# Kernel optimization log

Hardware: AMD Instinct MI355X
Metric: run time of the kernel (lower is better)

## Reference

```python
import jax, jax.numpy as jnp
import numpy as np

B = 64          # decode batch (one token per sequence)
HID = 4096      # hidden_size
HQ = 32         # num query heads
HKV = 8         # num kv heads (GQA, groups = 4)
D = 128         # head_dim
BS = 16         # block_size of paged KV cache
MAXB = 64       # max blocks per sequence -> max context 1024
MAXPOS = 4096   # rope table length
TOTAL_SLOTS = B * MAXB * BS


def setup_inputs() -> dict:
    key = jax.random.key(0)
    ks = jax.random.split(key, 10)
    hidden = jax.random.normal(ks[0], (B, 1, HID), jnp.float32)
    context_lens = jax.random.randint(ks[1], (B,), 512, BS * MAXB + 1).astype(jnp.int32)
    positions = (context_lens - 1).reshape(B, 1)  # decoding token position
    # each sequence owns a contiguous range of blocks
    block_tables = jnp.arange(B * MAXB, dtype=jnp.int32).reshape(B, MAXB)
    last = context_lens - 1
    slot_mapping = (block_tables[jnp.arange(B), last // BS] * BS + last % BS).astype(jnp.int32)
    inv_freq = 1.0 / (10000.0 ** (jnp.arange(0, D, 2, dtype=jnp.float32) / D))
    freqs = jnp.outer(jnp.arange(MAXPOS, dtype=jnp.float32), inv_freq)  # [MAXPOS, D/2]
    cos, sin = jnp.cos(freqs), jnp.sin(freqs)
    key_cache = jax.random.normal(ks[2], (TOTAL_SLOTS, HKV, D), jnp.float32) * 0.5
    value_cache = jax.random.normal(ks[3], (TOTAL_SLOTS, HKV, D), jnp.float32) * 0.5
    Wq = jax.random.normal(ks[4], (HQ * D, HID), jnp.float32) * 0.02
    Wk = jax.random.normal(ks[5], (HKV * D, HID), jnp.float32) * 0.02
    Wv = jax.random.normal(ks[6], (HKV * D, HID), jnp.float32) * 0.02
    Wo = jax.random.normal(ks[7], (HID, HQ * D), jnp.float32) * 0.02
    return dict(hidden=hidden, positions=positions, cos=cos, sin=sin,
                key_cache=key_cache, value_cache=value_cache,
                slot_mapping=slot_mapping, block_tables=block_tables,
                context_lens=context_lens, Wq=Wq, Wk=Wk, Wv=Wv, Wo=Wo)


def reference(hidden, positions, cos, sin, key_cache, value_cache,
              slot_mapping, block_tables, context_lens, Wq, Wk, Wv, Wo):
    b, s, _ = hidden.shape  # s == 1 (paged decode path)
    q = (hidden @ Wq.T).reshape(b, s, HQ, D)
    k = (hidden @ Wk.T).reshape(b, s, HKV, D)
    v = (hidden @ Wv.T).reshape(b, s, HKV, D)
    # rotary embedding (half-split convention)
    c = cos[positions][:, :, None, :]  # [b,s,1,D/2]
    sn = sin[positions][:, :, None, :]
    def rope(x):
        x1, x2 = jnp.split(x, 2, axis=-1)
        return jnp.concatenate([x1 * c - x2 * sn, x2 * c + x1 * sn], axis=-1)
    q, k = rope(q), rope(k)
    # scatter current token's K/V into the paged cache via slot_mapping
    kc = key_cache.at[slot_mapping].set(k.reshape(-1, HKV, D))
    vc = value_cache.at[slot_mapping].set(v.reshape(-1, HKV, D))
    # gather each sequence's KV via block tables
    T = MAXB * BS
    t = jnp.arange(T)
    slots = block_tables[:, t // BS] * BS + (t % BS)  # [b, T]
    keys = kc[slots]   # [b, T, HKV, D]
    vals = vc[slots]   # [b, T, HKV, D]
    # GQA attention, q has one token per sequence
    G = HQ // HKV
    qg = q.reshape(b, HKV, G, D)
    scores = jnp.einsum('bkgd,btkd->bkgt', qg, keys) / jnp.sqrt(jnp.float32(D))
    mask = t[None, :] < context_lens[:, None]  # [b, T]
    scores = jnp.where(mask[:, None, None, :], scores, -jnp.inf)
    p = jax.nn.softmax(scores, axis=-1)
    out = jnp.einsum('bkgt,btkd->bkgd', p, vals).reshape(b, 1, HQ * D)
    return out @ Wo.T
```

## Files before the change

### kernel.cpp

```cpp
#include <hip/hip_runtime.h>
#include <hip/hip_bf16.h>

#define B_    64
#define HID_  4096
#define HQ_   32
#define HKV_  8
#define D_    128
#define BS_   16
#define MAXB_ 64

#define KS      16
#define KCHUNK  (HID_ / KS)
#define QKV_ROWS 6144
#define O_ROWS   4096
#define SPLITS  16

#define REGION_SZ ((size_t)KS * QKV_ROWS * 64)
#define QKVF_SZ  ((size_t)64 * 6144)
#define XB_SZ    ((size_t)HID_ * 64)

typedef __attribute__((ext_vector_type(8))) short bf16x8;
typedef __attribute__((ext_vector_type(4))) float f32x4;

__device__ inline unsigned short f2bf(float x) {
  __hip_bfloat16 h = __float2bfloat16(x);
  union { __hip_bfloat16 b; unsigned short u; } v; v.b = h;
  return v.u;
}
__device__ inline float bf2f(unsigned short h) {
  union { float f; unsigned u; } v; v.u = ((unsigned)h) << 16;
  return v.f;
}

__global__ __launch_bounds__(256) void convert_x(
    const float* __restrict__ X, unsigned short* __restrict__ XBhi,
    unsigned short* __restrict__ XBlo)
{
  int idx = blockIdx.x * 256 + threadIdx.x;
  int kg = idx >> 6, b = idx & 63;
  const float* xp = X + (size_t)b * HID_ + kg * 8;
  float4 a = *(const float4*)xp, c = *(const float4*)(xp + 4);
  float xs[8] = {a.x, a.y, a.z, a.w, c.x, c.y, c.z, c.w};
  unsigned short hi[8], lo[8];
  #pragma unroll
  for (int j = 0; j < 8; ++j) {
    hi[j] = f2bf(xs[j]);
    lo[j] = f2bf(xs[j] - bf2f(hi[j]));
  }
  *(uint4*)(XBhi + (size_t)idx * 8) = *(const uint4*)hi;
  *(uint4*)(XBlo + (size_t)idx * 8) = *(const uint4*)lo;
}

__global__ __launch_bounds__(256, 4) void gemm_mfma(
    const float* __restrict__ W0, const float* __restrict__ W1,
    const float* __restrict__ W2,
    const unsigned short* __restrict__ XBhi,
    const unsigned short* __restrict__ XBlo,
    int split1, int split2, int rows_total, float* __restrict__ part)
{
  const int tid = threadIdx.x;
  const int l   = tid & 63;
  const int w   = tid >> 6;
  const int r0  = blockIdx.x * 128 + w * 32;
  const int k0  = blockIdx.y * KCHUNK;

  const float* W; int rloc;
  if (r0 < split1)      { W = W0; rloc = r0; }
  else if (r0 < split2) { W = W1; rloc = r0 - split1; }
  else                  { W = W2; rloc = r0 - split2; }

  const int lm = l & 15;
  const int lk = l >> 4;

  const float* wp0 = W + (size_t)(rloc + lm) * HID_ + k0 + lk * 8;
  const float* wp1 = wp0 + (size_t)16 * HID_;
  const unsigned short* bh = XBhi + ((size_t)(k0 / 8 + lk) * 64 + lm) * 8;
  const unsigned short* bl = XBlo + ((size_t)(k0 / 8 + lk) * 64 + lm) * 8;

  f32x4 acc[2][4];
  #pragma unroll
  for (int rt = 0; rt < 2; ++rt)
    #pragma unroll
    for (int ct = 0; ct < 4; ++ct)
      #pragma unroll
      for (int i = 0; i < 4; ++i) acc[rt][ct][i] = 0.f;

  #pragma unroll 4
  for (int ks = 0; ks < KCHUNK / 32; ++ks) {
    bf16x8 Bh[4], Bl[4];
    #pragma unroll
    for (int ct = 0; ct < 4; ++ct) {
      Bh[ct] = *(const bf16x8*)(bh + (size_t)ks * 2048 + ct * 128);
      Bl[ct] = *(const bf16x8*)(bl + (size_t)ks * 2048 + ct * 128);
    }
    #pragma unroll
    for (int rt = 0; rt < 2; ++rt) {
      const float* wp = (rt ? wp1 : wp0) + ks * 32;
      float4 a0 = *(const float4*)wp;
      float4 a1 = *(const float4*)(wp + 4);
      float xs[8] = {a0.x, a0.y, a0.z, a0.w, a1.x, a1.y, a1.z, a1.w};
      bf16x8 Ah, Al;
      #pragma unroll
      for (int j = 0; j < 8; ++j) {
        unsigned short h = f2bf(xs[j]);
        Ah[j] = (short)h;
        Al[j] = (short)f2bf(xs[j] - bf2f(h));
      }
      #pragma unroll
      for (int ct = 0; ct < 4; ++ct) {
        acc[rt][ct] = __builtin_amdgcn_mfma_f32_16x16x32_bf16(Ah, Bh[ct], acc[rt][ct], 0, 0, 0);
        acc[rt][ct] = __builtin_amdgcn_mfma_f32_16x16x32_bf16(Al, Bh[ct], acc[rt][ct], 0, 0, 0);
        acc[rt][ct] = __builtin_amdgcn_mfma_f32_16x16x32_bf16(Ah, Bl[ct], acc[rt][ct], 0, 0, 0);
      }
    }
  }

  #pragma unroll
  for (int rt = 0; rt < 2; ++rt)
    #pragma unroll
    for (int ct = 0; ct < 4; ++ct) {
      int row = r0 + rt * 16 + lk * 4;
      int bat = ct * 16 + lm;
      #pragma unroll
      for (int i = 0; i < 4; ++i)
        part[((size_t)blockIdx.y * rows_total + row + i) * 64 + bat] = acc[rt][ct][i];
    }
}

__global__ __launch_bounds__(256) void reduce_rope(
    const float* __restrict__ part, const float* __restrict__ cosT,
    const float* __restrict__ sinT, const int* __restrict__ positions,
    float* __restrict__ qkvf)
{
  const int bb  = threadIdx.x & 63;
  const int cid = blockIdx.x * 4 + (threadIdx.x >> 6);
  const int pos = positions[bb];

  if (cid < 2048) {
    const int hq = cid >> 6, d0 = cid & 63;
    const int r1 = hq * 128 + d0;
    float x1 = 0.f, x2 = 0.f;
    #pragma unroll 8
    for (int ks = 0; ks < KS; ++ks) {
      x1 += part[((size_t)ks * QKV_ROWS + r1) * 64 + bb];
      x2 += part[((size_t)ks * QKV_ROWS + r1 + 64) * 64 + bb];
    }
    float c = cosT[pos * 64 + d0], s = sinT[pos * 64 + d0];
    const float scale = 0.08838834764831843f;
    qkvf[(size_t)(bb * 32 + hq) * 128 + d0]      = (x1 * c - x2 * s) * scale;
    qkvf[(size_t)(bb * 32 + hq) * 128 + d0 + 64] = (x2 * c + x1 * s) * scale;
  } else if (cid < 2560) {
    const int c2 = cid - 2048;
    const int kh = c2 >> 6, d0 = c2 & 63;
    const int r1 = 4096 + kh * 128 + d0;
    float x1 = 0.f, x2 = 0.f;
    #pragma unroll 8
    for (int ks = 0; ks < KS; ++ks) {
      x1 += part[((size_t)ks * QKV_ROWS + r1) * 64 + bb];
      x2 += part[((size_t)ks * QKV_ROWS + r1 + 64) * 64 + bb];
    }
    float c = cosT[pos * 64 + d0], s = sinT[pos * 64 + d0];
    qkvf[262144 + (size_t)(bb * 8 + kh) * 128 + d0]      = x1 * c - x2 * s;
    qkvf[262144 + (size_t)(bb * 8 + kh) * 128 + d0 + 64] = x2 * c + x1 * s;
  } else {
    const int c2 = cid - 2560;
    const int kh = c2 >> 6, d0 = c2 & 63;
    const int r1 = 5120 + kh * 128 + d0;
    float x1 = 0.f, x2 = 0.f;
    #pragma unroll 8
    for (int ks = 0; ks < KS; ++ks) {
      x1 += part[((size_t)ks * QKV_ROWS + r1) * 64 + bb];
      x2 += part[((size_t)ks * QKV_ROWS + r1 + 64) * 64 + bb];
    }
    qkvf[327680 + (size_t)(bb * 8 + kh) * 128 + d0]      = x1;
    qkvf[327680 + (size_t)(bb * 8 + kh) * 128 + d0 + 64] = x2;
  }
}

__global__ __launch_bounds__(256, 4) void attn_split(
    const float* __restrict__ qkvf, const float* __restrict__ kcache,
    const float* __restrict__ vcache, const int* __restrict__ btab,
    const int* __restrict__ ctxlen,
    float* __restrict__ part_o,
    float* __restrict__ part_ml)
{
  const int bid = blockIdx.x;
  const int s   = bid & (SPLITS - 1);
  const int bh  = bid >> 4;
  const int b = bh >> 3, h = bh & 7;
  const int ctx   = ctxlen[b];
  const int chunk = (ctx + SPLITS - 1) / SPLITS;
  const int t0 = s * chunk;
  const int t1 = min(ctx, t0 + chunk);
  const int last = ctx - 1;
  const int tEnd = min(t1, last);

  const int tid  = threadIdx.x;
  const int half = tid >> 5;
  const int d4   = tid & 31;

  __shared__ int   sblk[8];
  __shared__ float wm[4][4], wl[4][4];
  __shared__ float wacc[4][4][128];

  const int blk0 = t0 >> 4;
  if (tid < 8) {
    int ib = blk0 + tid;
    sblk[tid] = (ib < MAXB_) ? btab[b * MAXB_ + ib] : 0;
  }
  __syncthreads();

  float4 qf[4];
  #pragma unroll
  for (int g = 0; g < 4; ++g)
    qf[g] = *(const float4*)(qkvf + (size_t)(b * 32 + h * 4 + g) * 128 + d4 * 4);

  float m[4], l[4], acc[4][4];
  #pragma unroll
  for (int g = 0; g < 4; ++g) {
    m[g] = -1e30f; l[g] = 0.f;
    #pragma unroll
    for (int j = 0; j < 4; ++j) acc[g][j] = 0.f;
  }

  for (int t = t0 + half; t < tEnd; t += 8) {
    int slot = sblk[(t >> 4) - blk0] * BS_ + (t & 15);
    const float* base = kcache + ((size_t)slot * HKV_ + h) * D_ + d4 * 4;
    const float* vbas = vcache + ((size_t)slot * HKV_ + h) * D_ + d4 * 4;
    float4 kv = *(const float4*)base;
    float4 vv = *(const float4*)vbas;

    float p0 = qf[0].x * kv.x + qf[0].y * kv.y + qf[0].z * kv.z + qf[0].w * kv.w;
    float p1 = qf[1].x * kv.x + qf[1].y * kv.y + qf[1].z * kv.z + qf[1].w * kv.w;
    float p2 = qf[2].x * kv.x + qf[2].y * kv.y + qf[2].z * kv.z + qf[2].w * kv.w;
    float p3 = qf[3].x * kv.x + qf[3].y * kv.y + qf[3].z * kv.z + qf[3].w * kv.w;
    #pragma unroll
    for (int mm = 16; mm >= 1; mm >>= 1) {
      p0 += __shfl_xor(p0, mm);
      p1 += __shfl_xor(p1, mm);
      p2 += __shfl_xor(p2, mm);
      p3 += __shfl_xor(p3, mm);
    }
    float pg[4] = {p0, p1, p2, p3};
    #pragma unroll
    for (int g = 0; g < 4; ++g) {
      float nm = fmaxf(m[g], pg[g]);
      float sc = __expf(m[g] - nm);
      float pe = __expf(pg[g] - nm);
      l[g] = l[g] * sc + pe;
      acc[g][0] = acc[g][0] * sc + pe * vv.x;
      acc[g][1] = acc[g][1] * sc + pe * vv.y;
      acc[g][2] = acc[g][2] * sc + pe * vv.z;
      acc[g][3] = acc[g][3] * sc + pe * vv.w;
      m[g] = nm;
    }
  }

  if (t1 > last && half == ((last - t0) & 7)) {
    const float* kp = qkvf + 262144 + (size_t)(b * 8 + h) * 128 + d4 * 4;
    const float* vp = qkvf + 327680 + (size_t)(b * 8 + h) * 128 + d4 * 4;
    float4 kv = *(const float4*)kp;
    float4 vv = *(const float4*)vp;
    float p0 = qf[0].x * kv.x + qf[0].y * kv.y + qf[0].z * kv.z + qf[0].w * kv.w;
    float p1 = qf[1].x * kv.x + qf[1].y * kv.y + qf[1].z * kv.z + qf[1].w * kv.w;
    float p2 = qf[2].x * kv.x + qf[2].y * kv.y + qf[2].z * kv.z + qf[2].w * kv.w;
    float p3 = qf[3].x * kv.x + qf[3].y * kv.y + qf[3].z * kv.z + qf[3].w * kv.w;
    #pragma unroll
    for (int mm = 16; mm >= 1; mm >>= 1) {
      p0 += __shfl_xor(p0, mm);
      p1 += __shfl_xor(p1, mm);
      p2 += __shfl_xor(p2, mm);
      p3 += __shfl_xor(p3, mm);
    }
    float pg[4] = {p0, p1, p2, p3};
    #pragma unroll
    for (int g = 0; g < 4; ++g) {
      float nm = fmaxf(m[g], pg[g]);
      float sc = __expf(m[g] - nm);
      float pe = __expf(pg[g] - nm);
      l[g] = l[g] * sc + pe;
      acc[g][0] = acc[g][0] * sc + pe * vv.x;
      acc[g][1] = acc[g][1] * sc + pe * vv.y;
      acc[g][2] = acc[g][2] * sc + pe * vv.z;
      acc[g][3] = acc[g][3] * sc + pe * vv.w;
      m[g] = nm;
    }
  }

  #pragma unroll
  for (int g = 0; g < 4; ++g) {
    float om = __shfl_xor(m[g], 32);
    float ol = __shfl_xor(l[g], 32);
    float M  = fmaxf(m[g], om);
    float s0 = __expf(m[g] - M);
    float s1 = __expf(om - M);
    l[g] = l[g] * s0 + ol * s1;
    #pragma unroll
    for (int j = 0; j < 4; ++j) {
      float oa = __shfl_xor(acc[g][j], 32);
      acc[g][j] = acc[g][j] * s0 + oa * s1;
    }
    m[g] = M;
  }
  if ((tid & 32) == 0) {
    int wv = tid >> 6;
    if (d4 == 0) {
      #pragma unroll
      for (int g = 0; g < 4; ++g) { wm[wv][g] = m[g]; wl[wv][g] = l[g]; }
    }
    #pragma unroll
    for (int g = 0; g < 4; ++g)
      #pragma unroll
      for (int j = 0; j < 4; ++j)
        wacc[wv][g][d4 * 4 + j] = acc[g][j];
  }
  __syncthreads();

  for (int idx = tid; idx < 512; idx += 256) {
    int g = idx >> 7, d = idx & 127;
    float M4 = fmaxf(fmaxf(wm[0][g], wm[1][g]), fmaxf(wm[2][g], wm[3][g]));
    float e0 = __expf(wm[0][g] - M4), e1 = __expf(wm[1][g] - M4);
    float e2 = __expf(wm[2][g] - M4), e3 = __expf(wm[3][g] - M4);
    float num = wacc[0][g][d] * e0 + wacc[1][g][d] * e1
              + wacc[2][g][d] * e2 + wacc[3][g][d] * e3;
    part_o[(size_t)bid * 512 + idx] = num;
    if (d == 0) {
      float lt = wl[0][g] * e0 + wl[1][g] * e1 + wl[2][g] * e2 + wl[3][g] * e3;
      part_ml[(size_t)bid * 8 + g * 2]     = M4;
      part_ml[(size_t)bid * 8 + g * 2 + 1] = lt;
    }
  }
}

__global__ __launch_bounds__(256) void attn_combine_xb(
    const float* __restrict__ part_o, const float* __restrict__ part_ml,
    unsigned short* __restrict__ XBhi, unsigned short* __restrict__ XBlo)
{
  const int bh = blockIdx.x;
  const int b = bh >> 3, h = bh & 7;
  const int tid = threadIdx.x;

  __shared__ float Sg[SPLITS][4];
  __shared__ float Dg[4];

  if (tid < 64) {
    int s = tid >> 2, g = tid & 3;
    float m = part_ml[((size_t)bh * SPLITS + s) * 8 + g * 2];
    float l = part_ml[((size_t)bh * SPLITS + s) * 8 + g * 2 + 1];
    float M = m;
    #pragma unroll
    for (int k = 4; k <= 32; k <<= 1) M = fmaxf(M, __shfl_xor(M, k));
    float scl = __expf(m - M);
    float dl = l * scl;
    #pragma unroll
    for (int k = 4; k <= 32; k <<= 1) dl += __shfl_xor(dl, k);
    Sg[s][g] = scl;
    if (s == 0) Dg[g] = dl;
  }
  __syncthreads();

  for (int idx = tid; idx < 512; idx += 256) {
    int g = idx >> 7, d = idx & 127;
    float num = 0.f;
    #pragma unroll
    for (int s = 0; s < SPLITS; ++s)
      num += Sg[s][g] * part_o[((size_t)bh * SPLITS + s) * 512 + idx];
    float val = num / Dg[g];
    int col = (h * 4 + g) * 128 + d;
    int kg = col >> 3, j = col & 7;
    unsigned short hi = f2bf(val);
    unsigned short lo = f2bf(val - bf2f(hi));
    XBhi[((size_t)kg * 64 + b) * 8 + j] = hi;
    XBlo[((size_t)kg * 64 + b) * 8 + j] = lo;
  }
}

__global__ __launch_bounds__(256) void reduce_out_t(
    const float* __restrict__ part, float* __restrict__ out)
{
  __shared__ float t[64][65];
  const int i0 = blockIdx.x * 64;
  const int lane = threadIdx.x & 63, q = threadIdx.x >> 6;

  #pragma unroll
  for (int rr = q; rr < 64; rr += 4) {
    float s = 0.f;
    #pragma unroll 8
    for (int ks = 0; ks < KS; ++ks)
      s += part[((size_t)ks * O_ROWS + i0 + rr) * 64 + lane];
    t[rr][lane] = s;
  }
  __syncthreads();
  #pragma unroll
  for (int rr = q; rr < 64; rr += 4)
    out[(size_t)rr * O_ROWS + i0 + lane] = t[lane][rr];
}

extern "C" void kernel_launch(void* const* d_in, const int* in_sizes, int n_in,
                              void* d_out, int out_size, void* d_ws, size_t ws_size,
                              hipStream_t stream)
{
  (void)in_sizes; (void)n_in; (void)out_size; (void)ws_size;
  const float* hidden    = (const float*)d_in[0];
  const int*   positions = (const int*)d_in[1];
  const float* cosT      = (const float*)d_in[2];
  const float* sinT      = (const float*)d_in[3];
  const float* kcache    = (const float*)d_in[4];
  const float* vcache    = (const float*)d_in[5];
  const int*   btab      = (const int*)d_in[7];
  const int*   ctx       = (const int*)d_in[8];
  const float* Wq        = (const float*)d_in[9];
  const float* Wk        = (const float*)d_in[10];
  const float* Wv        = (const float*)d_in[11];
  const float* Wo        = (const float*)d_in[12];
  float* out = (float*)d_out;

  float* ws      = (float*)d_ws;
  float* region  = ws;
  float* qkvf    = region + REGION_SZ;
  unsigned short* XBhi = (unsigned short*)(qkvf + QKVF_SZ);
  unsigned short* XBlo = XBhi + XB_SZ;
  float* part1   = region;
  float* part_o  = region;
  float* part_ml = region + (size_t)B_ * HKV_ * SPLITS * 512;
  float* part3   = region;

  convert_x<<<128, 256, 0, stream>>>(hidden, XBhi, XBlo);
  gemm_mfma<<<dim3(QKV_ROWS / 128, KS), 256, 0, stream>>>(
      Wq, Wk, Wv, XBhi, XBlo, 4096, 5120, QKV_ROWS, part1);
  reduce_rope<<<768, 256, 0, stream>>>(part1, cosT, sinT, positions, qkvf);
  attn_split<<<B_ * HKV_ * SPLITS, 256, 0, stream>>>(
      qkvf, kcache, vcache, btab, ctx, part_o, part_ml);
  attn_combine_xb<<<B_ * HKV_, 256, 0, stream>>>(part_o, part_ml, XBhi, XBlo);
  gemm_mfma<<<dim3(O_ROWS / 128, KS), 256, 0, stream>>>(
      Wo, Wo, Wo, XBhi, XBlo, O_ROWS, O_ROWS, O_ROWS, part3);
  reduce_out_t<<<O_ROWS / 64, 256, 0, stream>>>(part3, out);
}
```

Baseline: 185.2 us.

## Map KV heads to half-waves in attn_split and drop intra-block softmax merge

Each attention block now covers all 8 KV heads of one sequence split, with one 32-lane group per head, instead of one block per (sequence, head, split) with 8 token lanes. Each group walks its token chunk serially, so the shuffle/LDS cross-lane softmax merge and the __syncthreads disappear, and partial results are written straight out. Launched blocks drop by a factor of 8 (1024 instead of 8192), and each thread has a longer serial loop with less token-level parallelism for hiding memory latency. The combine kernel is rewritten to stage m/l in shared memory and compute the max and sum with 4 threads.

```diff
diff --git a/kernel.cpp b/kernel.cpp
--- a/kernel.cpp
+++ b/kernel.cpp
@@ -186,8 +186,7 @@
 {
   const int bid = blockIdx.x;
   const int s   = bid & (SPLITS - 1);
-  const int bh  = bid >> 4;
-  const int b = bh >> 3, h = bh & 7;
+  const int b   = bid >> 4;
   const int ctx   = ctxlen[b];
   const int chunk = (ctx + SPLITS - 1) / SPLITS;
   const int t0 = s * chunk;
@@ -195,14 +194,11 @@
   const int last = ctx - 1;
   const int tEnd = min(t1, last);
 
-  const int tid  = threadIdx.x;
-  const int half = tid >> 5;
-  const int d4   = tid & 31;
-
-  __shared__ int   sblk[8];
-  __shared__ float wm[4][4], wl[4][4];
-  __shared__ float wacc[4][4][128];
-
+  const int tid = threadIdx.x;
+  const int h   = tid >> 5;
+  const int d4  = tid & 31;
+
+  __shared__ int sblk[8];
   const int blk0 = t0 >> 4;
   if (tid < 8) {
     int ib = blk0 + tid;
@@ -223,12 +219,13 @@
     for (int j = 0; j < 4; ++j) acc[g][j] = 0.f;
   }
 
-  for (int t = t0 + half; t < tEnd; t += 8) {
+  #pragma unroll 2
+  for (int t = t0; t < tEnd; ++t) {
     int slot = sblk[(t >> 4) - blk0] * BS_ + (t & 15);
-    const float* base = kcache + ((size_t)slot * HKV_ + h) * D_ + d4 * 4;
-    const float* vbas = vcache + ((size_t)slot * HKV_ + h) * D_ + d4 * 4;
-    float4 kv = *(const float4*)base;
-    float4 vv = *(const float4*)vbas;
+    const float* kp = kcache + ((size_t)slot * HKV_ + h) * D_ + d4 * 4;
+    const float* vp = vcache + ((size_t)slot * HKV_ + h) * D_ + d4 * 4;
+    float4 kv = *(const float4*)kp;
+    float4 vv = *(const float4*)vp;
 
     float p0 = qf[0].x * kv.x + qf[0].y * kv.y + qf[0].z * kv.z + qf[0].w * kv.w;
     float p1 = qf[1].x * kv.x + qf[1].y * kv.y + qf[1].z * kv.z + qf[1].w * kv.w;
@@ -256,7 +253,7 @@
     }
   }
 
-  if (t1 > last && half == ((last - t0) & 7)) {
+  if (t0 <= last && t1 > last) {
     const float* kp = qkvf + 262144 + (size_t)(b * 8 + h) * 128 + d4 * 4;
     const float* vp = qkvf + 327680 + (size_t)(b * 8 + h) * 128 + d4 * 4;
     float4 kv = *(const float4*)kp;
@@ -287,48 +284,16 @@
     }
   }
 
-  #pragma unroll
-  for (int g = 0; g < 4; ++g) {
-    float om = __shfl_xor(m[g], 32);
-    float ol = __shfl_xor(l[g], 32);
-    float M  = fmaxf(m[g], om);
-    float s0 = __expf(m[g] - M);
-    float s1 = __expf(om - M);
-    l[g] = l[g] * s0 + ol * s1;
-    #pragma unroll
-    for (int j = 0; j < 4; ++j) {
-      float oa = __shfl_xor(acc[g][j], 32);
-      acc[g][j] = acc[g][j] * s0 + oa * s1;
-    }
-    m[g] = M;
-  }
-  if ((tid & 32) == 0) {
-    int wv = tid >> 6;
-    if (d4 == 0) {
-      #pragma unroll
-      for (int g = 0; g < 4; ++g) { wm[wv][g] = m[g]; wl[wv][g] = l[g]; }
-    }
-    #pragma unroll
-    for (int g = 0; g < 4; ++g)
-      #pragma unroll
-      for (int j = 0; j < 4; ++j)
-        wacc[wv][g][d4 * 4 + j] = acc[g][j];
-  }
-  __syncthreads();
-
-  for (int idx = tid; idx < 512; idx += 256) {
-    int g = idx >> 7, d = idx & 127;
-    float M4 = fmaxf(fmaxf(wm[0][g], wm[1][g]), fmaxf(wm[2][g], wm[3][g]));
-    float e0 = __expf(wm[0][g] - M4), e1 = __expf(wm[1][g] - M4);
-    float e2 = __expf(wm[2][g] - M4), e3 = __expf(wm[3][g] - M4);
-    float num = wacc[0][g][d] * e0 + wacc[1][g][d] * e1
-              + wacc[2][g][d] * e2 + wacc[3][g][d] * e3;
-    part_o[(size_t)bid * 512 + idx] = num;
-    if (d == 0) {
-      float lt = wl[0][g] * e0 + wl[1][g] * e1 + wl[2][g] * e2 + wl[3][g] * e3;
-      part_ml[(size_t)bid * 8 + g * 2]     = M4;
-      part_ml[(size_t)bid * 8 + g * 2 + 1] = lt;
-    }
+  float* po = part_o + ((size_t)(b * 8 + h) * SPLITS + s) * 512;
+  #pragma unroll
+  for (int g = 0; g < 4; ++g)
+    #pragma unroll
+    for (int j = 0; j < 4; ++j)
+      po[g * 128 + d4 * 4 + j] = acc[g][j];
+  if (d4 == 0) {
+    float* pm = part_ml + ((size_t)(b * 8 + h) * SPLITS + s) * 8;
+    #pragma unroll
+    for (int g = 0; g < 4; ++g) { pm[g * 2] = m[g]; pm[g * 2 + 1] = l[g]; }
   }
 }
 
@@ -340,22 +305,26 @@
   const int b = bh >> 3, h = bh & 7;
   const int tid = threadIdx.x;
 
+  __shared__ float ml[SPLITS][8];
   __shared__ float Sg[SPLITS][4];
   __shared__ float Dg[4];
 
-  if (tid < 64) {
-    int s = tid >> 2, g = tid & 3;
-    float m = part_ml[((size_t)bh * SPLITS + s) * 8 + g * 2];
-    float l = part_ml[((size_t)bh * SPLITS + s) * 8 + g * 2 + 1];
-    float M = m;
-    #pragma unroll
-    for (int k = 4; k <= 32; k <<= 1) M = fmaxf(M, __shfl_xor(M, k));
-    float scl = __expf(m - M);
-    float dl = l * scl;
-    #pragma unroll
-    for (int k = 4; k <= 32; k <<= 1) dl += __shfl_xor(dl, k);
-    Sg[s][g] = scl;
-    if (s == 0) Dg[g] = dl;
+  if (tid < SPLITS * 8)
+    ml[tid >> 3][tid & 7] = part_ml[(size_t)bh * SPLITS * 8 + tid];
+  __syncthreads();
+
+  if (tid < 4) {
+    float M = -1e30f;
+    #pragma unroll
+    for (int s = 0; s < SPLITS; ++s) M = fmaxf(M, ml[s][tid * 2]);
+    float D = 0.f;
+    #pragma unroll
+    for (int s = 0; s < SPLITS; ++s) {
+      float e = __expf(ml[s][tid * 2] - M);
+      Sg[s][tid] = e;
+      D += e * ml[s][tid * 2 + 1];
+    }
+    Dg[tid] = D;
   }
   __syncthreads();
 
@@ -429,7 +398,7 @@
   gemm_mfma<<<dim3(QKV_ROWS / 128, KS), 256, 0, stream>>>(
       Wq, Wk, Wv, XBhi, XBlo, 4096, 5120, QKV_ROWS, part1);
   reduce_rope<<<768, 256, 0, stream>>>(part1, cosT, sinT, positions, qkvf);
-  attn_split<<<B_ * HKV_ * SPLITS, 256, 0, stream>>>(
+  attn_split<<<B_ * SPLITS, 256, 0, stream>>>(
       qkvf, kcache, vcache, btab, ctx, part_o, part_ml);
   attn_combine_xb<<<B_ * HKV_, 256, 0, stream>>>(part_o, part_ml, XBhi, XBlo);
   gemm_mfma<<<dim3(O_ROWS / 128, KS), 256, 0, stream>>>(
```

Measured after the change: 192.4 us. +3.9%, slower.
